# Performance work log

Hardware: AMD Instinct MI355X
Metric: run time of the kernel (lower is better)

Reference implementation:

```python
import jax, jax.numpy as jnp
import numpy as np

SEQ_LEN = 12
B = 1024
NG = 32            # scenes
G = B // NG        # pedestrians per scene
E = 64             # embedding_dim
H = 128            # h_dim
PP = 512           # mlp_pre_pool hidden
BOT = 1024         # bottleneck_dim
MLPD = 1024        # mlp_dim


def _w(key, fan_in, shape):
    return jax.random.normal(key, shape, jnp.float32) / np.sqrt(fan_in)


def setup_inputs():
    key = jax.random.key(0)
    ks = jax.random.split(key, 16)
    starts = jnp.arange(NG, dtype=jnp.int32) * G
    inp = {
        'last_pos': jax.random.normal(ks[0], (B, 2), jnp.float32),
        'last_pos_rel': jax.random.normal(ks[1], (B, 2), jnp.float32) * 0.1,
        'decoder_h': jax.random.normal(ks[2], (1, B, H), jnp.float32) * 0.1,
        'decoder_c': jax.random.normal(ks[3], (1, B, H), jnp.float32) * 0.1,
        'seq_start_end': jnp.stack([starts, starts + G], axis=1),
        'W_emb': _w(ks[4], 2, (2, E)), 'b_emb': jnp.zeros((E,), jnp.float32),
        'W_ih': _w(ks[5], E, (4 * H, E)), 'b_ih': jnp.zeros((4 * H,), jnp.float32),
        'W_hh': _w(ks[6], H, (4 * H, H)), 'b_hh': jnp.zeros((4 * H,), jnp.float32),
        'W_h2p': _w(ks[7], H, (H, 2)), 'b_h2p': jnp.zeros((2,), jnp.float32),
        'W_sp': _w(ks[8], 2, (2, E)), 'b_sp': jnp.zeros((E,), jnp.float32),
        'W_pp1': _w(ks[9], E + H, (E + H, PP)), 'b_pp1': jnp.zeros((PP,), jnp.float32),
        'W_pp2': _w(ks[10], PP, (PP, BOT)), 'b_pp2': jnp.zeros((BOT,), jnp.float32),
        'W_m1': _w(ks[11], H + BOT, (H + BOT, MLPD)), 'b_m1': jnp.zeros((MLPD,), jnp.float32),
        'W_m2': _w(ks[12], MLPD, (MLPD, H)), 'b_m2': jnp.zeros((H,), jnp.float32),
    }
    return inp


def _forward(last_pos, last_pos_rel, h0, c0,
             W_emb, b_emb, W_ih, b_ih, W_hh, b_hh, W_h2p, b_h2p,
             W_sp, b_sp, W_pp1, b_pp1, W_pp2, b_pp2, W_m1, b_m1, W_m2, b_m2):
    relu = jax.nn.relu

    def pool_net(h, pos):
        # PoolHiddenNet over NG contiguous equal-size groups of G peds.
        hg = h.reshape(NG, G, H)
        pg = pos.reshape(NG, G, 2)
        # rel[g, i, j] = pos_j - pos_i  (matches repeat/tile ordering in torch code)
        rel = pg[:, None, :, :] - pg[:, :, None, :]          # [NG,G,G,2]
        emb = rel @ W_sp + b_sp                               # [NG,G,G,E]
        hj = jnp.broadcast_to(hg[:, None, :, :], (NG, G, G, H))
        x = jnp.concatenate([emb, hj], axis=-1)               # [NG,G,G,E+H]
        x = relu(x @ W_pp1 + b_pp1)
        x = relu(x @ W_pp2 + b_pp2)                           # [NG,G,G,BOT]
        return jnp.max(x, axis=2).reshape(B, BOT)             # max over neighbors j

    def lstm_cell(x, h, c):
        gates = x @ W_ih.T + b_ih + h @ W_hh.T + b_hh
        i, f, g, o = jnp.split(gates, 4, axis=-1)
        c2 = jax.nn.sigmoid(f) * c + jax.nn.sigmoid(i) * jnp.tanh(g)
        h2 = jax.nn.sigmoid(o) * jnp.tanh(c2)
        return h2, c2

    dec_in0 = last_pos_rel @ W_emb + b_emb

    def step(carry, _):
        lp, din, h, c = carry
        h, c = lstm_cell(din, h, c)
        rel_pos = h @ W_h2p + b_h2p                           # [B,2]
        curr_pos = rel_pos + lp
        pool_h = pool_net(h, curr_pos)                        # [B,BOT]
        hcat = jnp.concatenate([h, pool_h], axis=1)
        h = relu(relu(hcat @ W_m1 + b_m1) @ W_m2 + b_m2)      # refreshed decoder_h
        din = rel_pos @ W_emb + b_emb
        return (curr_pos, din, h, c), rel_pos

    (_, _, h_fin, _), pred = jax.lax.scan(
        step, (last_pos, dec_in0, h0, c0), None, length=SEQ_LEN)
    return pred, h_fin[None]                                  # [T,B,2], [1,B,H]


def reference(last_pos, last_pos_rel, decoder_h, decoder_c, seq_start_end,
              W_emb, b_emb, W_ih, b_ih, W_hh, b_hh, W_h2p, b_h2p,
              W_sp, b_sp, W_pp1, b_pp1, W_pp2, b_pp2, W_m1, b_m1, W_m2, b_m2):
    del seq_start_end  # uniform contiguous groups encoded statically (NG, G)
    return _forward(last_pos, last_pos_rel, decoder_h[0], decoder_c[0],
                    W_emb, b_emb, W_ih, b_ih, W_hh, b_hh, W_h2p, b_h2p,
                    W_sp, b_sp, W_pp1, b_pp1, W_pp2, b_pp2, W_m1, b_m1, W_m2, b_m2)
```

## Files before the change

kernel.cpp:

```cpp
#include <hip/hip_runtime.h>
#include <math.h>

#define T_SEQ 12

typedef __bf16 bf16x8 __attribute__((ext_vector_type(8)));
typedef float f32x4 __attribute__((ext_vector_type(4)));
typedef unsigned short u16x8 __attribute__((ext_vector_type(8)));

static __device__ __forceinline__ unsigned short bf16bits(float x) {
  return __builtin_bit_cast(unsigned short, (__bf16)x);
}

enum : int {
  OFF_LP    = 0,
  OFF_DIN   = 2048,
  OFF_C     = 198656,
  OFF_HDEC  = 329728,
  OFF_WC    = 460800,
  OFF_BC    = 461824,
  OFF_PW    = 462336,
  OFF_AA    = 986624,
  OFF_WP2T  = 1510912,
  OFF_WM1T  = 1773056,
  OFF_HCATB = 2362880,
  OFF_WM2TB = 2952704,
  OFF_MIDB  = 3018240,
  OFF_WIHT  = 3542528,
  OFF_WHHT  = 3575296,
  OFF_WFRAG = 3640832
};

#define SWZP(byte, row) ((byte) ^ (((row) & 7) << 4))

__global__ __launch_bounds__(256) void k_setup(
    const float* __restrict__ last_pos, const float* __restrict__ lpr,
    const float* __restrict__ dh, const float* __restrict__ dc,
    const float* __restrict__ W_emb, const float* __restrict__ b_emb,
    float* __restrict__ lp, float* __restrict__ din,
    float* __restrict__ h_dec, float* __restrict__ c) {
  int idx = blockIdx.x * 256 + threadIdx.x;
  if (idx < 2048) lp[idx] = last_pos[idx];
  h_dec[idx] = dh[idx];
  c[idx] = dc[idx];
  if (idx < 65536) {
    int b = idx >> 6, e = idx & 63;
    din[idx] = lpr[b*2] * W_emb[e] + lpr[b*2+1] * W_emb[64+e] + b_emb[e];
  }
}

__global__ __launch_bounds__(256) void k_wc(
    const float* __restrict__ W_sp, const float* __restrict__ b_sp,
    const float* __restrict__ W_pp1, const float* __restrict__ b_pp1,
    float* __restrict__ Wc, float* __restrict__ bc) {
  int n = blockIdx.x * 256 + threadIdx.x;
  if (n >= 512) return;
  float a0 = 0.f, a1 = 0.f, ab = 0.f;
#pragma unroll 8
  for (int k = 0; k < 64; k++) {
    float w = W_pp1[k*512 + n];
    a0 += W_sp[k] * w;
    a1 += W_sp[64+k] * w;
    ab += b_sp[k] * w;
  }
  Wc[n] = a0; Wc[512+n] = a1; bc[n] = ab + b_pp1[n];
}

__global__ __launch_bounds__(256) void k_tcvt(
    const float* __restrict__ src, unsigned short* __restrict__ dst,
    int R, int C) {
  __shared__ float t[32][33];
  const int bx = blockIdx.x * 32, by = blockIdx.y * 32;
  const int tx = threadIdx.x & 31, ty = threadIdx.x >> 5;
#pragma unroll
  for (int i = 0; i < 32; i += 8) t[ty+i][tx] = src[(size_t)(by+ty+i)*C + bx+tx];
  __syncthreads();
#pragma unroll
  for (int i = 0; i < 32; i += 8)
    dst[(size_t)(bx+ty+i)*R + by+tx] = bf16bits(t[tx][ty+i]);
}

__global__ __launch_bounds__(256) void k_t32(
    const float* __restrict__ src, float* __restrict__ dst, int R, int C) {
  __shared__ float t[32][33];
  const int bx = blockIdx.x * 32, by = blockIdx.y * 32;
  const int tx = threadIdx.x & 31, ty = threadIdx.x >> 5;
#pragma unroll
  for (int i = 0; i < 32; i += 8) t[ty+i][tx] = src[(size_t)(by+ty+i)*C + bx+tx];
  __syncthreads();
#pragma unroll
  for (int i = 0; i < 32; i += 8)
    dst[(size_t)(bx+ty+i)*R + by+tx] = t[tx][ty+i];
}

__global__ __launch_bounds__(256) void k_frag(
    const unsigned short* __restrict__ Wp2t, unsigned short* __restrict__ Wfrag) {
  const int tid = blockIdx.x * 256 + threadIdx.x;
  const int fid = tid >> 6, l = tid & 63;
  const int nbb = fid >> 4, ks = fid & 15;
  u16x8 v = *(const u16x8*)(Wp2t + (size_t)(nbb*16 + (l & 15))*512 +
                            ks*32 + (l >> 4)*8);
  *(u16x8*)(Wfrag + (size_t)tid*8) = v;
}

__global__ __launch_bounds__(512) void k_step1(
    float* __restrict__ din, const float* __restrict__ h_dec,
    float* __restrict__ cst, unsigned short* __restrict__ hcatB,
    float* __restrict__ lp, float* __restrict__ pred,
    const float* __restrict__ Wiht, const float* __restrict__ b_ih,
    const float* __restrict__ Whht, const float* __restrict__ b_hh,
    const float* __restrict__ W_h2p, const float* __restrict__ b_h2p,
    const float* __restrict__ W_emb, const float* __restrict__ b_emb,
    const float* __restrict__ W1b, const float* __restrict__ Wc,
    const float* __restrict__ bc,
    float* __restrict__ PW, float* __restrict__ Aa, int t) {
  const int b0 = blockIdx.x * 4;
  const int tid = threadIdx.x;
  __shared__ float xh[4*192];
  __shared__ float gl[4*512];
  __shared__ float hbuf[4*128];
  __shared__ float relS[8], curS[8];

  for (int i = tid; i < 768; i += 512) {
    int r = i / 192, k = i - r*192;
    xh[i] = (k < 64) ? din[(b0+r)*64 + k] : h_dec[(b0+r)*128 + k - 64];
  }
  __syncthreads();
  {
    const int n = tid;
    float bias = b_ih[n] + b_hh[n];
    float acc[4] = {bias, bias, bias, bias};
#pragma unroll 8
    for (int k = 0; k < 64; k++) {
      float wv = Wiht[k*512 + n];
#pragma unroll
      for (int r = 0; r < 4; r++) acc[r] += xh[r*192 + k] * wv;
    }
#pragma unroll 8
    for (int k = 0; k < 128; k++) {
      float wv = Whht[k*512 + n];
#pragma unroll
      for (int r = 0; r < 4; r++) acc[r] += xh[r*192 + 64 + k] * wv;
    }
#pragma unroll
    for (int r = 0; r < 4; r++) gl[r*512 + n] = acc[r];
  }
  __syncthreads();
  {
    int r = tid >> 7, hh = tid & 127;
    float ig = gl[r*512 + hh],       fg = gl[r*512 + 128 + hh];
    float gg = gl[r*512 + 256 + hh], og = gl[r*512 + 384 + hh];
    ig = 1.f/(1.f+expf(-ig)); fg = 1.f/(1.f+expf(-fg));
    gg = tanhf(gg);           og = 1.f/(1.f+expf(-og));
    int row = b0 + r;
    float c2 = fg * cst[row*128 + hh] + ig * gg;
    float h2 = og * tanhf(c2);
    cst[row*128 + hh] = c2;
    hbuf[r*128 + hh] = h2;
    hcatB[(size_t)row*1152 + hh] = bf16bits(h2);
  }
  __syncthreads();
  if (tid < 128) {
    int r = tid >> 5, col = (tid >> 4) & 1, l16 = tid & 15;
    float s = 0.f;
    for (int k = l16; k < 128; k += 16) s += hbuf[r*128 + k] * W_h2p[k*2 + col];
#pragma unroll
    for (int off = 8; off > 0; off >>= 1) s += __shfl_xor(s, off);
    if (l16 == 0) {
      float rel = s + b_h2p[col];
      float old = lp[(b0+r)*2 + col];
      relS[r*2 + col] = rel;
      curS[r*2 + col] = old + rel;
      lp[(b0+r)*2 + col] = old + rel;
      pred[t*2048 + (b0+r)*2 + col] = rel;
    }
  }
  __syncthreads();
  if (tid < 256) {
    int r = tid >> 6, e = tid & 63;
    din[(b0+r)*64 + e] = relS[r*2]*W_emb[e] + relS[r*2+1]*W_emb[64+e] + b_emb[e];
  }
  {
    const int n = tid;
    float acc[4] = {0.f, 0.f, 0.f, 0.f};
#pragma unroll 4
    for (int k = 0; k < 128; k++) {
      float wv = W1b[k*512 + n];
#pragma unroll
      for (int r = 0; r < 4; r++) acc[r] += hbuf[r*128 + k] * wv;
    }
    float wc0 = Wc[n], wc1 = Wc[512+n], bcv = bc[n];
#pragma unroll
    for (int r = 0; r < 4; r++) {
      float pw = curS[r*2]*wc0 + curS[r*2+1]*wc1;
      PW[(size_t)(b0+r)*512 + n] = pw;
      Aa[(size_t)(b0+r)*512 + n] = acc[r] + pw + bcv;
    }
  }
}

__global__ __launch_bounds__(512) void k_pool8(
    const float* __restrict__ Aa, const float* __restrict__ PW,
    const unsigned short* __restrict__ Wfrag, const float* __restrict__ bp2,
    unsigned short* __restrict__ hcatB) {
  const int bid = blockIdx.x;
  const int mt = (bid >> 3) & 7;
  const int g  = (bid & 7) + ((bid >> 6) << 3);
  const int tid = threadIdx.x, lane = tid & 63, w = tid >> 6;
  const int wr = w >> 2, wc = w & 3;
  const int l15 = lane & 15, lhi = lane >> 4;
  __shared__ __align__(128) char lds[163840];
  char* As = lds;
  char* B0 = lds + 131072;
  char* B1 = lds + 131072 + 16384;

  {
    const int ke = lane * 8;
#pragma unroll 4
    for (int rr = 0; rr < 16; rr++) {
      const int r = rr * 8 + w;
      const int j = r & 31, ii = r >> 5;
      const float* aRow = Aa + (size_t)(g*32 + j)*512 + ke;
      const float* pRow = PW + (size_t)(g*32 + mt*4 + ii)*512 + ke;
      float4 a0 = *(const float4*)aRow;
      float4 a1 = *(const float4*)(aRow + 4);
      float4 p0 = *(const float4*)pRow;
      float4 p1 = *(const float4*)(pRow + 4);
      bf16x8 y;
      y[0] = (__bf16)fmaxf(a0.x - p0.x, 0.f);
      y[1] = (__bf16)fmaxf(a0.y - p0.y, 0.f);
      y[2] = (__bf16)fmaxf(a0.z - p0.z, 0.f);
      y[3] = (__bf16)fmaxf(a0.w - p0.w, 0.f);
      y[4] = (__bf16)fmaxf(a1.x - p1.x, 0.f);
      y[5] = (__bf16)fmaxf(a1.y - p1.y, 0.f);
      y[6] = (__bf16)fmaxf(a1.z - p1.z, 0.f);
      y[7] = (__bf16)fmaxf(a1.w - p1.w, 0.f);
      *(bf16x8*)(As + SWZP(r*1024 + lane*16, r)) = y;
    }
  }

  const int u0 = tid, u1 = tid + 512;
  const size_t gfo0 = (size_t)((u0 >> 6) * 16) * 512 + (u0 & 63) * 8;
  const size_t gfo1 = (size_t)((u1 >> 6) * 16) * 512 + (u1 & 63) * 8;

  {
    u16x8 s0 = *(const u16x8*)(Wfrag + gfo0);
    u16x8 s1 = *(const u16x8*)(Wfrag + gfo1);
    *(u16x8*)(B0 + u0*16) = s0;
    *(u16x8*)(B0 + u1*16) = s1;
  }
  u16x8 r0, r1;
  {
    const size_t base = (size_t)512;
    r0 = *(const u16x8*)(Wfrag + base + gfo0);
    r1 = *(const u16x8*)(Wfrag + base + gfo1);
  }
  __syncthreads();

  for (int nt = 0; nt < 4; nt++) {
    f32x4 acc[4][4] = {};
#pragma unroll 4
    for (int k0 = 0; k0 < 16; k0++) {
      const int q = nt*16 + k0;
      char* Bcur = (q & 1) ? B1 : B0;
      char* Bnxt = (q & 1) ? B0 : B1;
      if (q < 63) {
        *(u16x8*)(Bnxt + u0*16) = r0;
        *(u16x8*)(Bnxt + u1*16) = r1;
      }
      if (q < 62) {
        const int q2 = q + 2;
        const size_t base = (size_t)((q2 >> 4) * 256 + (q2 & 15)) * 512;
        r0 = *(const u16x8*)(Wfrag + base + gfo0);
        r1 = *(const u16x8*)(Wfrag + base + gfo1);
      }
      bf16x8 af[4], bfr[4];
#pragma unroll
      for (int mf = 0; mf < 4; mf++) {
        const int row = wr*64 + mf*16 + l15;
        af[mf] = *(const bf16x8*)(As + SWZP(row*1024 + k0*64 + lhi*16, row));
      }
#pragma unroll
      for (int nf = 0; nf < 4; nf++)
        bfr[nf] = *(const bf16x8*)(Bcur + (wc*4 + nf)*1024 + lane*16);
#pragma unroll
      for (int mf = 0; mf < 4; mf++)
#pragma unroll
        for (int nf = 0; nf < 4; nf++)
          acc[mf][nf] = __builtin_amdgcn_mfma_f32_16x16x32_bf16(
              af[mf], bfr[nf], acc[mf][nf], 0, 0, 0);
      __syncthreads();
    }
#pragma unroll
    for (int isub = 0; isub < 2; isub++)
#pragma unroll
      for (int nf = 0; nf < 4; nf++) {
        f32x4 v0 = acc[isub*2][nf], v1 = acc[isub*2 + 1][nf];
        float mx = fmaxf(fmaxf(fmaxf(v0[0], v0[1]), fmaxf(v0[2], v0[3])),
                         fmaxf(fmaxf(v1[0], v1[1]), fmaxf(v1[2], v1[3])));
        mx = fmaxf(mx, __shfl_xor(mx, 16));
        mx = fmaxf(mx, __shfl_xor(mx, 32));
        if (lane < 16) {
          const int n = nt*256 + wc*64 + nf*16 + lane;
          const int i = mt*4 + wr*2 + isub;
          hcatB[(size_t)(g*32 + i)*1152 + 128 + n] =
              bf16bits(fmaxf(mx + bp2[n], 0.f));
        }
      }
  }
}

__global__ __launch_bounds__(256) void k_m1k(
    const unsigned short* __restrict__ A, const unsigned short* __restrict__ Bw,
    const float* __restrict__ bias, unsigned short* __restrict__ outB) {
  const int nt = blockIdx.x, mt = blockIdx.y;
  const int tid = threadIdx.x, lane = tid & 63, w = tid >> 6;
  const int l15 = lane & 15, lhi = lane >> 4;
  __shared__ __align__(128) char lds[65536];
  const unsigned short* aSrc = A  + (size_t)(mt*64)*1152;
  const unsigned short* bSrc = Bw + (size_t)(nt*64)*1152;

  u16x8 rg[8];
#pragma unroll
  for (int p = 0; p < 8; p++) {
    const int u = tid + p*256;
    const int isB = u >> 10, v = u & 1023;
    const int row = v >> 4, slot = v & 15;
    u16x8 val = *(const u16x8*)((isB ? bSrc : aSrc) + (size_t)row*1152 + slot*8);
    *(u16x8*)(lds + isB*16384 + SWZP(row*256 + slot*16, row)) = val;
  }
#pragma unroll
  for (int p = 0; p < 8; p++) {
    const int u = tid + p*256;
    const int isB = u >> 10, v = u & 1023;
    const int row = v >> 4, slot = v & 15;
    rg[p] = *(const u16x8*)((isB ? bSrc : aSrc) + (size_t)row*1152 + 128 + slot*8);
  }
  __syncthreads();

  f32x4 acc[4][4] = {};
  for (int c = 0; c < 9; c++) {
    const int cur = (c & 1) * 32768;
    const int nxt = 32768 - cur;
    if (c < 8) {
#pragma unroll
      for (int p = 0; p < 8; p++) {
        const int u = tid + p*256;
        const int isB = u >> 10, v = u & 1023;
        const int row = v >> 4, slot = v & 15;
        *(u16x8*)(lds + nxt + isB*16384 + SWZP(row*256 + slot*16, row)) = rg[p];
      }
    }
    if (c < 7) {
#pragma unroll
      for (int p = 0; p < 8; p++) {
        const int u = tid + p*256;
        const int isB = u >> 10, v = u & 1023;
        const int row = v >> 4, slot = v & 15;
        rg[p] = *(const u16x8*)((isB ? bSrc : aSrc) + (size_t)row*1152 +
                                (c+2)*128 + slot*8);
      }
    }
    bf16x8 af[4], bf[4];
#pragma unroll
    for (int mf = 0; mf < 4; mf++) {
      const int row = mf*16 + l15;
      af[mf] = *(const bf16x8*)(lds + cur + SWZP(row*256 + w*64 + lhi*16, row));
    }
#pragma unroll
    for (int nf = 0; nf < 4; nf++) {
      const int row = nf*16 + l15;
      bf[nf] = *(const bf16x8*)(lds + cur + 16384 +
                                SWZP(row*256 + w*64 + lhi*16, row));
    }
#pragma unroll
    for (int mf = 0; mf < 4; mf++)
#pragma unroll
      for (int nf = 0; nf < 4; nf++)
        acc[mf][nf] = __builtin_amdgcn_mfma_f32_16x16x32_bf16(
            af[mf], bf[nf], acc[mf][nf], 0, 0, 0);
    __syncthreads();
  }

#pragma unroll
  for (int mf = 0; mf < 4; mf++)
#pragma unroll
    for (int nf = 0; nf < 4; nf++)
      *(f32x4*)(lds + w*16384 + (mf*4 + nf)*1024 + lane*16) = acc[mf][nf];
  __syncthreads();
#pragma unroll
  for (int pi = 0; pi < 4; pi++) {
    const int p = w*4 + pi;
    f32x4 s = *(const f32x4*)(lds + p*1024 + lane*16);
#pragma unroll
    for (int wv = 1; wv < 4; wv++) {
      f32x4 q = *(const f32x4*)(lds + wv*16384 + p*1024 + lane*16);
      s[0] += q[0]; s[1] += q[1]; s[2] += q[2]; s[3] += q[3];
    }
    const int col = nt*64 + (p & 3)*16 + l15;
    const float bv = bias[col];
#pragma unroll
    for (int r = 0; r < 4; r++) {
      const int row = mt*64 + (p >> 2)*16 + lhi*4 + r;
      outB[(size_t)row*1024 + col] = bf16bits(fmaxf(s[r] + bv, 0.f));
    }
  }
}

__global__ __launch_bounds__(256) void k_m2k(
    const unsigned short* __restrict__ A, const unsigned short* __restrict__ Bw,
    const float* __restrict__ bias, float* __restrict__ hd) {
  const int nt = blockIdx.x, mt = blockIdx.y;
  const int tid = threadIdx.x, lane = tid & 63, w = tid >> 6;
  const int l15 = lane & 15, lhi = lane >> 4;
  __shared__ __align__(128) char lds[49152];
  const unsigned short* aSrc = A  + (size_t)(mt*32)*1024;
  const unsigned short* bSrc = Bw + (size_t)(nt*64)*1024;

  u16x8 rg[6];
#pragma unroll
  for (int p = 0; p < 6; p++) {
    const int u = tid + p*256;
    const int isB = (u >= 512);
    const int v = isB ? (u - 512) : u;
    const int row = v >> 4, slot = v & 15;
    u16x8 val = *(const u16x8*)((isB ? bSrc : aSrc) + (size_t)row*1024 + slot*8);
    *(u16x8*)(lds + isB*8192 + SWZP(row*256 + slot*16, row)) = val;
  }
#pragma unroll
  for (int p = 0; p < 6; p++) {
    const int u = tid + p*256;
    const int isB = (u >= 512);
    const int v = isB ? (u - 512) : u;
    const int row = v >> 4, slot = v & 15;
    rg[p] = *(const u16x8*)((isB ? bSrc : aSrc) + (size_t)row*1024 + 128 + slot*8);
  }
  __syncthreads();

  f32x4 acc[2][4] = {};
  for (int c = 0; c < 8; c++) {
    const int cur = (c & 1) * 24576;
    const int nxt = 24576 - cur;
    if (c < 7) {
#pragma unroll
      for (int p = 0; p < 6; p++) {
        const int u = tid + p*256;
        const int isB = (u >= 512);
        const int v = isB ? (u - 512) : u;
        const int row = v >> 4, slot = v & 15;
        *(u16x8*)(lds + nxt + isB*8192 + SWZP(row*256 + slot*16, row)) = rg[p];
      }
    }
    if (c < 6) {
#pragma unroll
      for (int p = 0; p < 6; p++) {
        const int u = tid + p*256;
        const int isB = (u >= 512);
        const int v = isB ? (u - 512) : u;
        const int row = v >> 4, slot = v & 15;
        rg[p] = *(const u16x8*)((isB ? bSrc : aSrc) + (size_t)row*1024 +
                                (c+2)*128 + slot*8);
      }
    }
    bf16x8 af[2], bf[4];
#pragma unroll
    for (int mf = 0; mf < 2; mf++) {
      const int row = mf*16 + l15;
      af[mf] = *(const bf16x8*)(lds + cur + SWZP(row*256 + w*64 + lhi*16, row));
    }
#pragma unroll
    for (int nf = 0; nf < 4; nf++) {
      const int row = nf*16 + l15;
      bf[nf] = *(const bf16x8*)(lds + cur + 8192 +
                                SWZP(row*256 + w*64 + lhi*16, row));
    }
#pragma unroll
    for (int mf = 0; mf < 2; mf++)
#pragma unroll
      for (int nf = 0; nf < 4; nf++)
        acc[mf][nf] = __builtin_amdgcn_mfma_f32_16x16x32_bf16(
            af[mf], bf[nf], acc[mf][nf], 0, 0, 0);
    __syncthreads();
  }

#pragma unroll
  for (int mf = 0; mf < 2; mf++)
#pragma unroll
    for (int nf = 0; nf < 4; nf++)
      *(f32x4*)(lds + w*8192 + (mf*4 + nf)*1024 + lane*16) = acc[mf][nf];
  __syncthreads();
#pragma unroll
  for (int pi = 0; pi < 2; pi++) {
    const int p = w*2 + pi;
    f32x4 s = *(const f32x4*)(lds + p*1024 + lane*16);
#pragma unroll
    for (int wv = 1; wv < 4; wv++) {
      f32x4 q = *(const f32x4*)(lds + wv*8192 + p*1024 + lane*16);
      s[0] += q[0]; s[1] += q[1]; s[2] += q[2]; s[3] += q[3];
    }
    const int col = nt*64 + (p & 3)*16 + l15;
    const float bv = bias[col];
#pragma unroll
    for (int r = 0; r < 4; r++) {
      const int row = mt*32 + (p >> 2)*16 + lhi*4 + r;
      hd[(size_t)row*128 + col] = fmaxf(s[r] + bv, 0.f);
    }
  }
}

__global__ __launch_bounds__(256) void k_hfin(const float* __restrict__ h_dec,
                                              float* __restrict__ out) {
  int idx = blockIdx.x * 256 + threadIdx.x;
  if (idx < 131072) out[24576 + idx] = h_dec[idx];
}

extern "C" void kernel_launch(void* const* d_in, const int* in_sizes, int n_in,
                              void* d_out, int out_size, void* d_ws, size_t ws_size,
                              hipStream_t stream) {
  const float* last_pos = (const float*)d_in[0];
  const float* lpr      = (const float*)d_in[1];
  const float* dh       = (const float*)d_in[2];
  const float* dc       = (const float*)d_in[3];
  const float* W_emb = (const float*)d_in[5];
  const float* b_emb = (const float*)d_in[6];
  const float* W_ih  = (const float*)d_in[7];
  const float* b_ih  = (const float*)d_in[8];
  const float* W_hh  = (const float*)d_in[9];
  const float* b_hh  = (const float*)d_in[10];
  const float* W_h2p = (const float*)d_in[11];
  const float* b_h2p = (const float*)d_in[12];
  const float* W_sp  = (const float*)d_in[13];
  const float* b_sp  = (const float*)d_in[14];
  const float* W_pp1 = (const float*)d_in[15];
  const float* b_pp1 = (const float*)d_in[16];
  const float* W_pp2 = (const float*)d_in[17];
  const float* b_pp2 = (const float*)d_in[18];
  const float* W_m1  = (const float*)d_in[19];
  const float* b_m1  = (const float*)d_in[20];
  const float* W_m2  = (const float*)d_in[21];
  const float* b_m2  = (const float*)d_in[22];

  float* ws    = (float*)d_ws;
  float* lp    = ws + OFF_LP;
  float* din   = ws + OFF_DIN;
  float* cst   = ws + OFF_C;
  float* h_dec = ws + OFF_HDEC;
  float* Wc    = ws + OFF_WC;
  float* bc    = ws + OFF_BC;
  float* PW    = ws + OFF_PW;
  float* Aa    = ws + OFF_AA;
  unsigned short* Wp2t  = (unsigned short*)(ws + OFF_WP2T);
  unsigned short* Wm1t  = (unsigned short*)(ws + OFF_WM1T);
  unsigned short* hcatB = (unsigned short*)(ws + OFF_HCATB);
  unsigned short* Wm2tB = (unsigned short*)(ws + OFF_WM2TB);
  unsigned short* midB  = (unsigned short*)(ws + OFF_MIDB);
  float* Wiht  = ws + OFF_WIHT;
  float* Whht  = ws + OFF_WHHT;
  unsigned short* Wfrag = (unsigned short*)(ws + OFF_WFRAG);
  float* out   = (float*)d_out;

  k_setup<<<512, 256, 0, stream>>>(last_pos, lpr, dh, dc, W_emb, b_emb, lp, din, h_dec, cst);
  k_wc<<<2, 256, 0, stream>>>(W_sp, b_sp, W_pp1, b_pp1, Wc, bc);
  { dim3 gt(32, 16); k_tcvt<<<gt, 256, 0, stream>>>(W_pp2, Wp2t, 512, 1024); }
  { dim3 gt(32, 36); k_tcvt<<<gt, 256, 0, stream>>>(W_m1, Wm1t, 1152, 1024); }
  { dim3 gt(4, 32);  k_tcvt<<<gt, 256, 0, stream>>>(W_m2, Wm2tB, 1024, 128); }
  { dim3 gt(2, 16);  k_t32<<<gt, 256, 0, stream>>>(W_ih, Wiht, 512, 64); }
  { dim3 gt(4, 16);  k_t32<<<gt, 256, 0, stream>>>(W_hh, Whht, 512, 128); }
  k_frag<<<256, 256, 0, stream>>>(Wp2t, Wfrag);

  for (int t = 0; t < T_SEQ; t++) {
    k_step1<<<256, 512, 0, stream>>>(din, h_dec, cst, hcatB, lp, out,
                                     Wiht, b_ih, Whht, b_hh, W_h2p, b_h2p,
                                     W_emb, b_emb, W_pp1 + 64*512, Wc, bc,
                                     PW, Aa, t);
    k_pool8<<<256, 512, 0, stream>>>(Aa, PW, Wfrag, b_pp2, hcatB);
    { dim3 gm(16, 16); k_m1k<<<gm, 256, 0, stream>>>(hcatB, Wm1t, b_m1, midB); }
    { dim3 gm(2, 32);  k_m2k<<<gm, 256, 0, stream>>>(midB, Wm2tB, b_m2, h_dec); }
  }
  k_hfin<<<512, 256, 0, stream>>>(h_dec, out);
}
```

Baseline: 994.9 us.

## Fuse per-step kernels into one persistent cooperative kernel with grid syncs

Replaces the 48 per-timestep launches (LSTM step, pooling GEMM, two MLP GEMMs) and the final copy with one cooperative kernel of 256 blocks that loops over timesteps and uses grid.sync between stages. The m1/m2 GEMMs are re-tiled to fit the 256-block, 512-thread grid. The goal is to remove launch overhead and inter-kernel gaps. In exchange, each block must use 160KB LDS and only one block fits per CU, so the GEMM stages run with a fixed grid shape and grid-wide barriers, which may lower occupancy or efficiency for the smaller GEMMs.

```diff
diff --git a/kernel.cpp b/kernel.cpp
--- a/kernel.cpp
+++ b/kernel.cpp
@@ -1,5 +1,8 @@
 #include <hip/hip_runtime.h>
+#include <hip/hip_cooperative_groups.h>
 #include <math.h>
+
+namespace cg = cooperative_groups;
 
 #define T_SEQ 12
 
@@ -102,415 +105,404 @@
   *(u16x8*)(Wfrag + (size_t)tid*8) = v;
 }
 
-__global__ __launch_bounds__(512) void k_step1(
-    float* __restrict__ din, const float* __restrict__ h_dec,
-    float* __restrict__ cst, unsigned short* __restrict__ hcatB,
-    float* __restrict__ lp, float* __restrict__ pred,
-    const float* __restrict__ Wiht, const float* __restrict__ b_ih,
-    const float* __restrict__ Whht, const float* __restrict__ b_hh,
-    const float* __restrict__ W_h2p, const float* __restrict__ b_h2p,
-    const float* __restrict__ W_emb, const float* __restrict__ b_emb,
-    const float* __restrict__ W1b, const float* __restrict__ Wc,
-    const float* __restrict__ bc,
-    float* __restrict__ PW, float* __restrict__ Aa, int t) {
-  const int b0 = blockIdx.x * 4;
-  const int tid = threadIdx.x;
-  __shared__ float xh[4*192];
-  __shared__ float gl[4*512];
-  __shared__ float hbuf[4*128];
-  __shared__ float relS[8], curS[8];
-
-  for (int i = tid; i < 768; i += 512) {
-    int r = i / 192, k = i - r*192;
-    xh[i] = (k < 64) ? din[(b0+r)*64 + k] : h_dec[(b0+r)*128 + k - 64];
-  }
-  __syncthreads();
-  {
-    const int n = tid;
-    float bias = b_ih[n] + b_hh[n];
-    float acc[4] = {bias, bias, bias, bias};
-#pragma unroll 8
-    for (int k = 0; k < 64; k++) {
-      float wv = Wiht[k*512 + n];
-#pragma unroll
-      for (int r = 0; r < 4; r++) acc[r] += xh[r*192 + k] * wv;
-    }
-#pragma unroll 8
-    for (int k = 0; k < 128; k++) {
-      float wv = Whht[k*512 + n];
-#pragma unroll
-      for (int r = 0; r < 4; r++) acc[r] += xh[r*192 + 64 + k] * wv;
-    }
-#pragma unroll
-    for (int r = 0; r < 4; r++) gl[r*512 + n] = acc[r];
-  }
-  __syncthreads();
-  {
-    int r = tid >> 7, hh = tid & 127;
-    float ig = gl[r*512 + hh],       fg = gl[r*512 + 128 + hh];
-    float gg = gl[r*512 + 256 + hh], og = gl[r*512 + 384 + hh];
-    ig = 1.f/(1.f+expf(-ig)); fg = 1.f/(1.f+expf(-fg));
-    gg = tanhf(gg);           og = 1.f/(1.f+expf(-og));
-    int row = b0 + r;
-    float c2 = fg * cst[row*128 + hh] + ig * gg;
-    float h2 = og * tanhf(c2);
-    cst[row*128 + hh] = c2;
-    hbuf[r*128 + hh] = h2;
-    hcatB[(size_t)row*1152 + hh] = bf16bits(h2);
-  }
-  __syncthreads();
-  if (tid < 128) {
-    int r = tid >> 5, col = (tid >> 4) & 1, l16 = tid & 15;
-    float s = 0.f;
-    for (int k = l16; k < 128; k += 16) s += hbuf[r*128 + k] * W_h2p[k*2 + col];
-#pragma unroll
-    for (int off = 8; off > 0; off >>= 1) s += __shfl_xor(s, off);
-    if (l16 == 0) {
-      float rel = s + b_h2p[col];
-      float old = lp[(b0+r)*2 + col];
-      relS[r*2 + col] = rel;
-      curS[r*2 + col] = old + rel;
-      lp[(b0+r)*2 + col] = old + rel;
-      pred[t*2048 + (b0+r)*2 + col] = rel;
-    }
-  }
-  __syncthreads();
-  if (tid < 256) {
-    int r = tid >> 6, e = tid & 63;
-    din[(b0+r)*64 + e] = relS[r*2]*W_emb[e] + relS[r*2+1]*W_emb[64+e] + b_emb[e];
-  }
-  {
-    const int n = tid;
-    float acc[4] = {0.f, 0.f, 0.f, 0.f};
-#pragma unroll 4
-    for (int k = 0; k < 128; k++) {
-      float wv = W1b[k*512 + n];
-#pragma unroll
-      for (int r = 0; r < 4; r++) acc[r] += hbuf[r*128 + k] * wv;
-    }
-    float wc0 = Wc[n], wc1 = Wc[512+n], bcv = bc[n];
-#pragma unroll
-    for (int r = 0; r < 4; r++) {
-      float pw = curS[r*2]*wc0 + curS[r*2+1]*wc1;
-      PW[(size_t)(b0+r)*512 + n] = pw;
-      Aa[(size_t)(b0+r)*512 + n] = acc[r] + pw + bcv;
-    }
-  }
-}
-
-__global__ __launch_bounds__(512) void k_pool8(
-    const float* __restrict__ Aa, const float* __restrict__ PW,
-    const unsigned short* __restrict__ Wfrag, const float* __restrict__ bp2,
-    unsigned short* __restrict__ hcatB) {
+__global__ void __launch_bounds__(512)
+k_mega(float* din, float* cst, float* h_dec, unsigned short* hcatB,
+       float* lp, float* out,
+       const float* Wiht, const float* b_ih,
+       const float* Whht, const float* b_hh,
+       const float* W_h2p, const float* b_h2p,
+       const float* W_emb, const float* b_emb,
+       const float* W1b, const float* Wc, const float* bc,
+       float* PW, float* Aa,
+       const unsigned short* Wfrag, const float* bp2,
+       const unsigned short* Wm1t, const float* b_m1, unsigned short* midB,
+       const unsigned short* Wm2tB, const float* b_m2) {
+  cg::grid_group grid = cg::this_grid();
+  __shared__ __align__(128) char smem[163840];
   const int bid = blockIdx.x;
-  const int mt = (bid >> 3) & 7;
-  const int g  = (bid & 7) + ((bid >> 6) << 3);
-  const int tid = threadIdx.x, lane = tid & 63, w = tid >> 6;
-  const int wr = w >> 2, wc = w & 3;
-  const int l15 = lane & 15, lhi = lane >> 4;
-  __shared__ __align__(128) char lds[163840];
-  char* As = lds;
-  char* B0 = lds + 131072;
-  char* B1 = lds + 131072 + 16384;
-
-  {
-    const int ke = lane * 8;
-#pragma unroll 4
-    for (int rr = 0; rr < 16; rr++) {
-      const int r = rr * 8 + w;
-      const int j = r & 31, ii = r >> 5;
-      const float* aRow = Aa + (size_t)(g*32 + j)*512 + ke;
-      const float* pRow = PW + (size_t)(g*32 + mt*4 + ii)*512 + ke;
-      float4 a0 = *(const float4*)aRow;
-      float4 a1 = *(const float4*)(aRow + 4);
-      float4 p0 = *(const float4*)pRow;
-      float4 p1 = *(const float4*)(pRow + 4);
-      bf16x8 y;
-      y[0] = (__bf16)fmaxf(a0.x - p0.x, 0.f);
-      y[1] = (__bf16)fmaxf(a0.y - p0.y, 0.f);
-      y[2] = (__bf16)fmaxf(a0.z - p0.z, 0.f);
-      y[3] = (__bf16)fmaxf(a0.w - p0.w, 0.f);
-      y[4] = (__bf16)fmaxf(a1.x - p1.x, 0.f);
-      y[5] = (__bf16)fmaxf(a1.y - p1.y, 0.f);
-      y[6] = (__bf16)fmaxf(a1.z - p1.z, 0.f);
-      y[7] = (__bf16)fmaxf(a1.w - p1.w, 0.f);
-      *(bf16x8*)(As + SWZP(r*1024 + lane*16, r)) = y;
-    }
-  }
-
-  const int u0 = tid, u1 = tid + 512;
-  const size_t gfo0 = (size_t)((u0 >> 6) * 16) * 512 + (u0 & 63) * 8;
-  const size_t gfo1 = (size_t)((u1 >> 6) * 16) * 512 + (u1 & 63) * 8;
-
-  {
-    u16x8 s0 = *(const u16x8*)(Wfrag + gfo0);
-    u16x8 s1 = *(const u16x8*)(Wfrag + gfo1);
-    *(u16x8*)(B0 + u0*16) = s0;
-    *(u16x8*)(B0 + u1*16) = s1;
-  }
-  u16x8 r0, r1;
-  {
-    const size_t base = (size_t)512;
-    r0 = *(const u16x8*)(Wfrag + base + gfo0);
-    r1 = *(const u16x8*)(Wfrag + base + gfo1);
-  }
-  __syncthreads();
-
-  for (int nt = 0; nt < 4; nt++) {
-    f32x4 acc[4][4] = {};
-#pragma unroll 4
-    for (int k0 = 0; k0 < 16; k0++) {
-      const int q = nt*16 + k0;
-      char* Bcur = (q & 1) ? B1 : B0;
-      char* Bnxt = (q & 1) ? B0 : B1;
-      if (q < 63) {
-        *(u16x8*)(Bnxt + u0*16) = r0;
-        *(u16x8*)(Bnxt + u1*16) = r1;
-      }
-      if (q < 62) {
-        const int q2 = q + 2;
-        const size_t base = (size_t)((q2 >> 4) * 256 + (q2 & 15)) * 512;
-        r0 = *(const u16x8*)(Wfrag + base + gfo0);
-        r1 = *(const u16x8*)(Wfrag + base + gfo1);
-      }
-      bf16x8 af[4], bfr[4];
-#pragma unroll
-      for (int mf = 0; mf < 4; mf++) {
-        const int row = wr*64 + mf*16 + l15;
-        af[mf] = *(const bf16x8*)(As + SWZP(row*1024 + k0*64 + lhi*16, row));
-      }
-#pragma unroll
-      for (int nf = 0; nf < 4; nf++)
-        bfr[nf] = *(const bf16x8*)(Bcur + (wc*4 + nf)*1024 + lane*16);
-#pragma unroll
-      for (int mf = 0; mf < 4; mf++)
-#pragma unroll
-        for (int nf = 0; nf < 4; nf++)
-          acc[mf][nf] = __builtin_amdgcn_mfma_f32_16x16x32_bf16(
-              af[mf], bfr[nf], acc[mf][nf], 0, 0, 0);
-      __syncthreads();
-    }
-#pragma unroll
-    for (int isub = 0; isub < 2; isub++)
-#pragma unroll
-      for (int nf = 0; nf < 4; nf++) {
-        f32x4 v0 = acc[isub*2][nf], v1 = acc[isub*2 + 1][nf];
-        float mx = fmaxf(fmaxf(fmaxf(v0[0], v0[1]), fmaxf(v0[2], v0[3])),
-                         fmaxf(fmaxf(v1[0], v1[1]), fmaxf(v1[2], v1[3])));
-        mx = fmaxf(mx, __shfl_xor(mx, 16));
-        mx = fmaxf(mx, __shfl_xor(mx, 32));
-        if (lane < 16) {
-          const int n = nt*256 + wc*64 + nf*16 + lane;
-          const int i = mt*4 + wr*2 + isub;
-          hcatB[(size_t)(g*32 + i)*1152 + 128 + n] =
-              bf16bits(fmaxf(mx + bp2[n], 0.f));
-        }
-      }
-  }
-}
-
-__global__ __launch_bounds__(256) void k_m1k(
-    const unsigned short* __restrict__ A, const unsigned short* __restrict__ Bw,
-    const float* __restrict__ bias, unsigned short* __restrict__ outB) {
-  const int nt = blockIdx.x, mt = blockIdx.y;
   const int tid = threadIdx.x, lane = tid & 63, w = tid >> 6;
   const int l15 = lane & 15, lhi = lane >> 4;
-  __shared__ __align__(128) char lds[65536];
-  const unsigned short* aSrc = A  + (size_t)(mt*64)*1152;
-  const unsigned short* bSrc = Bw + (size_t)(nt*64)*1152;
-
-  u16x8 rg[8];
-#pragma unroll
-  for (int p = 0; p < 8; p++) {
-    const int u = tid + p*256;
-    const int isB = u >> 10, v = u & 1023;
-    const int row = v >> 4, slot = v & 15;
-    u16x8 val = *(const u16x8*)((isB ? bSrc : aSrc) + (size_t)row*1152 + slot*8);
-    *(u16x8*)(lds + isB*16384 + SWZP(row*256 + slot*16, row)) = val;
-  }
-#pragma unroll
-  for (int p = 0; p < 8; p++) {
-    const int u = tid + p*256;
-    const int isB = u >> 10, v = u & 1023;
-    const int row = v >> 4, slot = v & 15;
-    rg[p] = *(const u16x8*)((isB ? bSrc : aSrc) + (size_t)row*1152 + 128 + slot*8);
-  }
-  __syncthreads();
-
-  f32x4 acc[4][4] = {};
-  for (int c = 0; c < 9; c++) {
-    const int cur = (c & 1) * 32768;
-    const int nxt = 32768 - cur;
-    if (c < 8) {
-#pragma unroll
-      for (int p = 0; p < 8; p++) {
-        const int u = tid + p*256;
+
+  for (int t = 0; t < T_SEQ; t++) {
+    {
+      float* xh   = (float*)smem;
+      float* gl   = xh + 768;
+      float* hbuf = gl + 2048;
+      float* relS = hbuf + 512;
+      float* curS = relS + 8;
+      const int b0 = bid * 4;
+      for (int i = tid; i < 768; i += 512) {
+        int r = i / 192, k = i - r*192;
+        xh[i] = (k < 64) ? din[(b0+r)*64 + k] : h_dec[(b0+r)*128 + k - 64];
+      }
+      __syncthreads();
+      {
+        const int n = tid;
+        float bias = b_ih[n] + b_hh[n];
+        float acc[4] = {bias, bias, bias, bias};
+#pragma unroll 8
+        for (int k = 0; k < 64; k++) {
+          float wv = Wiht[k*512 + n];
+#pragma unroll
+          for (int r = 0; r < 4; r++) acc[r] += xh[r*192 + k] * wv;
+        }
+#pragma unroll 8
+        for (int k = 0; k < 128; k++) {
+          float wv = Whht[k*512 + n];
+#pragma unroll
+          for (int r = 0; r < 4; r++) acc[r] += xh[r*192 + 64 + k] * wv;
+        }
+#pragma unroll
+        for (int r = 0; r < 4; r++) gl[r*512 + n] = acc[r];
+      }
+      __syncthreads();
+      {
+        int r = tid >> 7, hh = tid & 127;
+        float ig = gl[r*512 + hh],       fg = gl[r*512 + 128 + hh];
+        float gg = gl[r*512 + 256 + hh], og = gl[r*512 + 384 + hh];
+        ig = 1.f/(1.f+expf(-ig)); fg = 1.f/(1.f+expf(-fg));
+        gg = tanhf(gg);           og = 1.f/(1.f+expf(-og));
+        int row = b0 + r;
+        float c2 = fg * cst[row*128 + hh] + ig * gg;
+        float h2 = og * tanhf(c2);
+        cst[row*128 + hh] = c2;
+        hbuf[r*128 + hh] = h2;
+        hcatB[(size_t)row*1152 + hh] = bf16bits(h2);
+      }
+      __syncthreads();
+      if (tid < 128) {
+        int r = tid >> 5, col = (tid >> 4) & 1, l16 = tid & 15;
+        float s = 0.f;
+        for (int k = l16; k < 128; k += 16) s += hbuf[r*128 + k] * W_h2p[k*2 + col];
+#pragma unroll
+        for (int off = 8; off > 0; off >>= 1) s += __shfl_xor(s, off);
+        if (l16 == 0) {
+          float rel = s + b_h2p[col];
+          float old = lp[(b0+r)*2 + col];
+          relS[r*2 + col] = rel;
+          curS[r*2 + col] = old + rel;
+          lp[(b0+r)*2 + col] = old + rel;
+          out[t*2048 + (b0+r)*2 + col] = rel;
+        }
+      }
+      __syncthreads();
+      if (tid < 256) {
+        int r = tid >> 6, e = tid & 63;
+        din[(b0+r)*64 + e] = relS[r*2]*W_emb[e] + relS[r*2+1]*W_emb[64+e] + b_emb[e];
+      }
+      {
+        const int n = tid;
+        float acc[4] = {0.f, 0.f, 0.f, 0.f};
+#pragma unroll 4
+        for (int k = 0; k < 128; k++) {
+          float wv = W1b[k*512 + n];
+#pragma unroll
+          for (int r = 0; r < 4; r++) acc[r] += hbuf[r*128 + k] * wv;
+        }
+        float wc0 = Wc[n], wc1 = Wc[512+n], bcv = bc[n];
+#pragma unroll
+        for (int r = 0; r < 4; r++) {
+          float pw = curS[r*2]*wc0 + curS[r*2+1]*wc1;
+          PW[(size_t)(b0+r)*512 + n] = pw;
+          Aa[(size_t)(b0+r)*512 + n] = acc[r] + pw + bcv;
+        }
+      }
+    }
+    grid.sync();
+
+    {
+      const int mt = (bid >> 3) & 7;
+      const int g  = (bid & 7) + ((bid >> 6) << 3);
+      const int wr = w >> 2, wcn = w & 3;
+      char* As = smem;
+      char* B0 = smem + 131072;
+      char* B1 = smem + 131072 + 16384;
+      {
+        const int ke = lane * 8;
+#pragma unroll 4
+        for (int rr = 0; rr < 16; rr++) {
+          const int r = rr * 8 + w;
+          const int j = r & 31, ii = r >> 5;
+          const float* aRow = Aa + (size_t)(g*32 + j)*512 + ke;
+          const float* pRow = PW + (size_t)(g*32 + mt*4 + ii)*512 + ke;
+          float4 a0 = *(const float4*)aRow;
+          float4 a1 = *(const float4*)(aRow + 4);
+          float4 p0 = *(const float4*)pRow;
+          float4 p1 = *(const float4*)(pRow + 4);
+          bf16x8 y;
+          y[0] = (__bf16)fmaxf(a0.x - p0.x, 0.f);
+          y[1] = (__bf16)fmaxf(a0.y - p0.y, 0.f);
+          y[2] = (__bf16)fmaxf(a0.z - p0.z, 0.f);
+          y[3] = (__bf16)fmaxf(a0.w - p0.w, 0.f);
+          y[4] = (__bf16)fmaxf(a1.x - p1.x, 0.f);
+          y[5] = (__bf16)fmaxf(a1.y - p1.y, 0.f);
+          y[6] = (__bf16)fmaxf(a1.z - p1.z, 0.f);
+          y[7] = (__bf16)fmaxf(a1.w - p1.w, 0.f);
+          *(bf16x8*)(As + SWZP(r*1024 + lane*16, r)) = y;
+        }
+      }
+      const int u0 = tid, u1 = tid + 512;
+      const size_t gfo0 = (size_t)((u0 >> 6) * 16) * 512 + (u0 & 63) * 8;
+      const size_t gfo1 = (size_t)((u1 >> 6) * 16) * 512 + (u1 & 63) * 8;
+      {
+        u16x8 s0 = *(const u16x8*)(Wfrag + gfo0);
+        u16x8 s1 = *(const u16x8*)(Wfrag + gfo1);
+        *(u16x8*)(B0 + u0*16) = s0;
+        *(u16x8*)(B0 + u1*16) = s1;
+      }
+      u16x8 r0, r1;
+      {
+        r0 = *(const u16x8*)(Wfrag + 512 + gfo0);
+        r1 = *(const u16x8*)(Wfrag + 512 + gfo1);
+      }
+      __syncthreads();
+      for (int nt2 = 0; nt2 < 4; nt2++) {
+        f32x4 acc[4][4] = {};
+        for (int k0 = 0; k0 < 16; k0++) {
+          const int q = nt2*16 + k0;
+          char* Bcur = (q & 1) ? B1 : B0;
+          char* Bnxt = (q & 1) ? B0 : B1;
+          if (q < 63) {
+            *(u16x8*)(Bnxt + u0*16) = r0;
+            *(u16x8*)(Bnxt + u1*16) = r1;
+          }
+          if (q < 62) {
+            const int q2 = q + 2;
+            const size_t base = (size_t)((q2 >> 4) * 256 + (q2 & 15)) * 512;
+            r0 = *(const u16x8*)(Wfrag + base + gfo0);
+            r1 = *(const u16x8*)(Wfrag + base + gfo1);
+          }
+          bf16x8 af[4], bfr[4];
+#pragma unroll
+          for (int mf = 0; mf < 4; mf++) {
+            const int row = wr*64 + mf*16 + l15;
+            af[mf] = *(const bf16x8*)(As + SWZP(row*1024 + k0*64 + lhi*16, row));
+          }
+#pragma unroll
+          for (int nf = 0; nf < 4; nf++)
+            bfr[nf] = *(const bf16x8*)(Bcur + (wcn*4 + nf)*1024 + lane*16);
+#pragma unroll
+          for (int mf = 0; mf < 4; mf++)
+#pragma unroll
+            for (int nf = 0; nf < 4; nf++)
+              acc[mf][nf] = __builtin_amdgcn_mfma_f32_16x16x32_bf16(
+                  af[mf], bfr[nf], acc[mf][nf], 0, 0, 0);
+          __syncthreads();
+        }
+#pragma unroll
+        for (int isub = 0; isub < 2; isub++)
+#pragma unroll
+          for (int nf = 0; nf < 4; nf++) {
+            f32x4 v0 = acc[isub*2][nf], v1 = acc[isub*2 + 1][nf];
+            float mx = fmaxf(fmaxf(fmaxf(v0[0], v0[1]), fmaxf(v0[2], v0[3])),
+                             fmaxf(fmaxf(v1[0], v1[1]), fmaxf(v1[2], v1[3])));
+            mx = fmaxf(mx, __shfl_xor(mx, 16));
+            mx = fmaxf(mx, __shfl_xor(mx, 32));
+            if (lane < 16) {
+              const int n = nt2*256 + wcn*64 + nf*16 + lane;
+              const int i = mt*4 + wr*2 + isub;
+              hcatB[(size_t)(g*32 + i)*1152 + 128 + n] =
+                  bf16bits(fmaxf(mx + bp2[n], 0.f));
+            }
+          }
+      }
+    }
+    grid.sync();
+
+    {
+      const int nt = bid & 15, mt = bid >> 4;
+      const unsigned short* aSrc = hcatB + (size_t)(mt*64)*1152;
+      const unsigned short* bSrc = Wm1t + (size_t)(nt*64)*1152;
+      const int wk = w >> 1, wn = w & 1;
+      u16x8 rg[4];
+#pragma unroll
+      for (int p = 0; p < 4; p++) {
+        const int u = tid + p*512;
         const int isB = u >> 10, v = u & 1023;
         const int row = v >> 4, slot = v & 15;
-        *(u16x8*)(lds + nxt + isB*16384 + SWZP(row*256 + slot*16, row)) = rg[p];
-      }
-    }
-    if (c < 7) {
-#pragma unroll
-      for (int p = 0; p < 8; p++) {
-        const int u = tid + p*256;
+        u16x8 val = *(const u16x8*)((isB ? bSrc : aSrc) + (size_t)row*1152 + slot*8);
+        *(u16x8*)(smem + isB*16384 + SWZP(row*256 + slot*16, row)) = val;
+      }
+#pragma unroll
+      for (int p = 0; p < 4; p++) {
+        const int u = tid + p*512;
         const int isB = u >> 10, v = u & 1023;
         const int row = v >> 4, slot = v & 15;
-        rg[p] = *(const u16x8*)((isB ? bSrc : aSrc) + (size_t)row*1152 +
-                                (c+2)*128 + slot*8);
+        rg[p] = *(const u16x8*)((isB ? bSrc : aSrc) + (size_t)row*1152 + 128 + slot*8);
+      }
+      __syncthreads();
+      f32x4 acc[4][2] = {};
+      for (int c = 0; c < 9; c++) {
+        const int cur = (c & 1) * 32768;
+        const int nxt = 32768 - cur;
+        if (c < 8) {
+#pragma unroll
+          for (int p = 0; p < 4; p++) {
+            const int u = tid + p*512;
+            const int isB = u >> 10, v = u & 1023;
+            const int row = v >> 4, slot = v & 15;
+            *(u16x8*)(smem + nxt + isB*16384 + SWZP(row*256 + slot*16, row)) = rg[p];
+          }
+        }
+        if (c < 7) {
+#pragma unroll
+          for (int p = 0; p < 4; p++) {
+            const int u = tid + p*512;
+            const int isB = u >> 10, v = u & 1023;
+            const int row = v >> 4, slot = v & 15;
+            rg[p] = *(const u16x8*)((isB ? bSrc : aSrc) + (size_t)row*1152 +
+                                    (c+2)*128 + slot*8);
+          }
+        }
+        bf16x8 af[4], bf[2];
+#pragma unroll
+        for (int mf = 0; mf < 4; mf++) {
+          const int row = mf*16 + l15;
+          af[mf] = *(const bf16x8*)(smem + cur +
+                                    SWZP(row*256 + wk*64 + lhi*16, row));
+        }
+#pragma unroll
+        for (int nf = 0; nf < 2; nf++) {
+          const int row = wn*32 + nf*16 + l15;
+          bf[nf] = *(const bf16x8*)(smem + cur + 16384 +
+                                    SWZP(row*256 + wk*64 + lhi*16, row));
+        }
+#pragma unroll
+        for (int mf = 0; mf < 4; mf++)
+#pragma unroll
+          for (int nf = 0; nf < 2; nf++)
+            acc[mf][nf] = __builtin_amdgcn_mfma_f32_16x16x32_bf16(
+                af[mf], bf[nf], acc[mf][nf], 0, 0, 0);
+        __syncthreads();
+      }
+#pragma unroll
+      for (int mf = 0; mf < 4; mf++)
+#pragma unroll
+        for (int nf = 0; nf < 2; nf++)
+          *(f32x4*)(smem + (w*8 + mf*2 + nf)*1024 + lane*16) = acc[mf][nf];
+      __syncthreads();
+#pragma unroll
+      for (int pi = 0; pi < 2; pi++) {
+        const int p = w*2 + pi;
+        const int mf = p >> 2, nfg = p & 3;
+        f32x4 s = {0.f, 0.f, 0.f, 0.f};
+#pragma unroll
+        for (int wkk = 0; wkk < 4; wkk++) {
+          const int src = (wkk*2 + (nfg >> 1))*8 + mf*2 + (nfg & 1);
+          f32x4 q = *(const f32x4*)(smem + src*1024 + lane*16);
+          s[0] += q[0]; s[1] += q[1]; s[2] += q[2]; s[3] += q[3];
+        }
+        const int col = nt*64 + nfg*16 + l15;
+        const float bv = b_m1[col];
+#pragma unroll
+        for (int r = 0; r < 4; r++) {
+          const int row = mt*64 + mf*16 + lhi*4 + r;
+          midB[(size_t)row*1024 + col] = bf16bits(fmaxf(s[r] + bv, 0.f));
+        }
       }
     }
-    bf16x8 af[4], bf[4];
-#pragma unroll
-    for (int mf = 0; mf < 4; mf++) {
-      const int row = mf*16 + l15;
-      af[mf] = *(const bf16x8*)(lds + cur + SWZP(row*256 + w*64 + lhi*16, row));
+    grid.sync();
+
+    if (bid < 64) {
+      const int nt = bid & 1, mt = bid >> 1;
+      const unsigned short* aSrc = midB  + (size_t)(mt*32)*1024;
+      const unsigned short* bSrc = Wm2tB + (size_t)(nt*64)*1024;
+      u16x8 rg[6];
+#pragma unroll
+      for (int p = 0; p < 6; p++) {
+        const int u = tid + p*512;
+        const int isB = (u >= 1024);
+        const int v = isB ? (u - 1024) : u;
+        const int row = v >> 5, slot = v & 31;
+        u16x8 val = *(const u16x8*)((isB ? bSrc : aSrc) + (size_t)row*1024 + slot*8);
+        *(u16x8*)(smem + isB*16384 + SWZP(row*512 + slot*16, row)) = val;
+      }
+#pragma unroll
+      for (int p = 0; p < 6; p++) {
+        const int u = tid + p*512;
+        const int isB = (u >= 1024);
+        const int v = isB ? (u - 1024) : u;
+        const int row = v >> 5, slot = v & 31;
+        rg[p] = *(const u16x8*)((isB ? bSrc : aSrc) + (size_t)row*1024 + 256 + slot*8);
+      }
+      __syncthreads();
+      f32x4 acc[2][4] = {};
+      for (int c = 0; c < 4; c++) {
+        const int cur = (c & 1) * 49152;
+        const int nxt = 49152 - cur;
+        if (c < 3) {
+#pragma unroll
+          for (int p = 0; p < 6; p++) {
+            const int u = tid + p*512;
+            const int isB = (u >= 1024);
+            const int v = isB ? (u - 1024) : u;
+            const int row = v >> 5, slot = v & 31;
+            *(u16x8*)(smem + nxt + isB*16384 + SWZP(row*512 + slot*16, row)) = rg[p];
+          }
+        }
+        if (c < 2) {
+#pragma unroll
+          for (int p = 0; p < 6; p++) {
+            const int u = tid + p*512;
+            const int isB = (u >= 1024);
+            const int v = isB ? (u - 1024) : u;
+            const int row = v >> 5, slot = v & 31;
+            rg[p] = *(const u16x8*)((isB ? bSrc : aSrc) + (size_t)row*1024 +
+                                    (c+2)*256 + slot*8);
+          }
+        }
+        bf16x8 af[2], bf[4];
+#pragma unroll
+        for (int mf = 0; mf < 2; mf++) {
+          const int row = mf*16 + l15;
+          af[mf] = *(const bf16x8*)(smem + cur +
+                                    SWZP(row*512 + w*64 + lhi*16, row));
+        }
+#pragma unroll
+        for (int nf = 0; nf < 4; nf++) {
+          const int row = nf*16 + l15;
+          bf[nf] = *(const bf16x8*)(smem + cur + 16384 +
+                                    SWZP(row*512 + w*64 + lhi*16, row));
+        }
+#pragma unroll
+        for (int mf = 0; mf < 2; mf++)
+#pragma unroll
+          for (int nf = 0; nf < 4; nf++)
+            acc[mf][nf] = __builtin_amdgcn_mfma_f32_16x16x32_bf16(
+                af[mf], bf[nf], acc[mf][nf], 0, 0, 0);
+        __syncthreads();
+      }
+#pragma unroll
+      for (int mf = 0; mf < 2; mf++)
+#pragma unroll
+        for (int nf = 0; nf < 4; nf++)
+          *(f32x4*)(smem + (w*8 + mf*4 + nf)*1024 + lane*16) = acc[mf][nf];
+      __syncthreads();
+      {
+        const int p = w;
+        const int mf = p >> 2, nf = p & 3;
+        f32x4 s = {0.f, 0.f, 0.f, 0.f};
+#pragma unroll
+        for (int wv = 0; wv < 8; wv++) {
+          f32x4 q = *(const f32x4*)(smem + (wv*8 + p)*1024 + lane*16);
+          s[0] += q[0]; s[1] += q[1]; s[2] += q[2]; s[3] += q[3];
+        }
+        const int col = nt*64 + nf*16 + l15;
+        const float bv = b_m2[col];
+#pragma unroll
+        for (int r = 0; r < 4; r++) {
+          const int row = mt*32 + mf*16 + lhi*4 + r;
+          h_dec[(size_t)row*128 + col] = fmaxf(s[r] + bv, 0.f);
+        }
+      }
     }
-#pragma unroll
-    for (int nf = 0; nf < 4; nf++) {
-      const int row = nf*16 + l15;
-      bf[nf] = *(const bf16x8*)(lds + cur + 16384 +
-                                SWZP(row*256 + w*64 + lhi*16, row));
-    }
-#pragma unroll
-    for (int mf = 0; mf < 4; mf++)
-#pragma unroll
-      for (int nf = 0; nf < 4; nf++)
-        acc[mf][nf] = __builtin_amdgcn_mfma_f32_16x16x32_bf16(
-            af[mf], bf[nf], acc[mf][nf], 0, 0, 0);
-    __syncthreads();
+    grid.sync();
   }
 
-#pragma unroll
-  for (int mf = 0; mf < 4; mf++)
-#pragma unroll
-    for (int nf = 0; nf < 4; nf++)
-      *(f32x4*)(lds + w*16384 + (mf*4 + nf)*1024 + lane*16) = acc[mf][nf];
-  __syncthreads();
-#pragma unroll
-  for (int pi = 0; pi < 4; pi++) {
-    const int p = w*4 + pi;
-    f32x4 s = *(const f32x4*)(lds + p*1024 + lane*16);
-#pragma unroll
-    for (int wv = 1; wv < 4; wv++) {
-      f32x4 q = *(const f32x4*)(lds + wv*16384 + p*1024 + lane*16);
-      s[0] += q[0]; s[1] += q[1]; s[2] += q[2]; s[3] += q[3];
-    }
-    const int col = nt*64 + (p & 3)*16 + l15;
-    const float bv = bias[col];
-#pragma unroll
-    for (int r = 0; r < 4; r++) {
-      const int row = mt*64 + (p >> 2)*16 + lhi*4 + r;
-      outB[(size_t)row*1024 + col] = bf16bits(fmaxf(s[r] + bv, 0.f));
-    }
+  {
+    const int idx = bid * 512 + tid;
+    out[24576 + idx] = h_dec[idx];
   }
-}
-
-__global__ __launch_bounds__(256) void k_m2k(
-    const unsigned short* __restrict__ A, const unsigned short* __restrict__ Bw,
-    const float* __restrict__ bias, float* __restrict__ hd) {
-  const int nt = blockIdx.x, mt = blockIdx.y;
-  const int tid = threadIdx.x, lane = tid & 63, w = tid >> 6;
-  const int l15 = lane & 15, lhi = lane >> 4;
-  __shared__ __align__(128) char lds[49152];
-  const unsigned short* aSrc = A  + (size_t)(mt*32)*1024;
-  const unsigned short* bSrc = Bw + (size_t)(nt*64)*1024;
-
-  u16x8 rg[6];
-#pragma unroll
-  for (int p = 0; p < 6; p++) {
-    const int u = tid + p*256;
-    const int isB = (u >= 512);
-    const int v = isB ? (u - 512) : u;
-    const int row = v >> 4, slot = v & 15;
-    u16x8 val = *(const u16x8*)((isB ? bSrc : aSrc) + (size_t)row*1024 + slot*8);
-    *(u16x8*)(lds + isB*8192 + SWZP(row*256 + slot*16, row)) = val;
-  }
-#pragma unroll
-  for (int p = 0; p < 6; p++) {
-    const int u = tid + p*256;
-    const int isB = (u >= 512);
-    const int v = isB ? (u - 512) : u;
-    const int row = v >> 4, slot = v & 15;
-    rg[p] = *(const u16x8*)((isB ? bSrc : aSrc) + (size_t)row*1024 + 128 + slot*8);
-  }
-  __syncthreads();
-
-  f32x4 acc[2][4] = {};
-  for (int c = 0; c < 8; c++) {
-    const int cur = (c & 1) * 24576;
-    const int nxt = 24576 - cur;
-    if (c < 7) {
-#pragma unroll
-      for (int p = 0; p < 6; p++) {
-        const int u = tid + p*256;
-        const int isB = (u >= 512);
-        const int v = isB ? (u - 512) : u;
-        const int row = v >> 4, slot = v & 15;
-        *(u16x8*)(lds + nxt + isB*8192 + SWZP(row*256 + slot*16, row)) = rg[p];
-      }
-    }
-    if (c < 6) {
-#pragma unroll
-      for (int p = 0; p < 6; p++) {
-        const int u = tid + p*256;
-        const int isB = (u >= 512);
-        const int v = isB ? (u - 512) : u;
-        const int row = v >> 4, slot = v & 15;
-        rg[p] = *(const u16x8*)((isB ? bSrc : aSrc) + (size_t)row*1024 +
-                                (c+2)*128 + slot*8);
-      }
-    }
-    bf16x8 af[2], bf[4];
-#pragma unroll
-    for (int mf = 0; mf < 2; mf++) {
-      const int row = mf*16 + l15;
-      af[mf] = *(const bf16x8*)(lds + cur + SWZP(row*256 + w*64 + lhi*16, row));
-    }
-#pragma unroll
-    for (int nf = 0; nf < 4; nf++) {
-      const int row = nf*16 + l15;
-      bf[nf] = *(const bf16x8*)(lds + cur + 8192 +
-                                SWZP(row*256 + w*64 + lhi*16, row));
-    }
-#pragma unroll
-    for (int mf = 0; mf < 2; mf++)
-#pragma unroll
-      for (int nf = 0; nf < 4; nf++)
-        acc[mf][nf] = __builtin_amdgcn_mfma_f32_16x16x32_bf16(
-            af[mf], bf[nf], acc[mf][nf], 0, 0, 0);
-    __syncthreads();
-  }
-
-#pragma unroll
-  for (int mf = 0; mf < 2; mf++)
-#pragma unroll
-    for (int nf = 0; nf < 4; nf++)
-      *(f32x4*)(lds + w*8192 + (mf*4 + nf)*1024 + lane*16) = acc[mf][nf];
-  __syncthreads();
-#pragma unroll
-  for (int pi = 0; pi < 2; pi++) {
-    const int p = w*2 + pi;
-    f32x4 s = *(const f32x4*)(lds + p*1024 + lane*16);
-#pragma unroll
-    for (int wv = 1; wv < 4; wv++) {
-      f32x4 q = *(const f32x4*)(lds + wv*8192 + p*1024 + lane*16);
-      s[0] += q[0]; s[1] += q[1]; s[2] += q[2]; s[3] += q[3];
-    }
-    const int col = nt*64 + (p & 3)*16 + l15;
-    const float bv = bias[col];
-#pragma unroll
-    for (int r = 0; r < 4; r++) {
-      const int row = mt*32 + (p >> 2)*16 + lhi*4 + r;
-      hd[(size_t)row*128 + col] = fmaxf(s[r] + bv, 0.f);
-    }
-  }
-}
-
-__global__ __launch_bounds__(256) void k_hfin(const float* __restrict__ h_dec,
-                                              float* __restrict__ out) {
-  int idx = blockIdx.x * 256 + threadIdx.x;
-  if (idx < 131072) out[24576 + idx] = h_dec[idx];
 }
 
 extern "C" void kernel_launch(void* const* d_in, const int* in_sizes, int n_in,
@@ -557,6 +549,7 @@
   float* Whht  = ws + OFF_WHHT;
   unsigned short* Wfrag = (unsigned short*)(ws + OFF_WFRAG);
   float* out   = (float*)d_out;
+  const float* W1b = W_pp1 + 64*512;
 
   k_setup<<<512, 256, 0, stream>>>(last_pos, lpr, dh, dc, W_emb, b_emb, lp, din, h_dec, cst);
   k_wc<<<2, 256, 0, stream>>>(W_sp, b_sp, W_pp1, b_pp1, Wc, bc);
@@ -567,14 +560,16 @@
   { dim3 gt(4, 16);  k_t32<<<gt, 256, 0, stream>>>(W_hh, Whht, 512, 128); }
   k_frag<<<256, 256, 0, stream>>>(Wp2t, Wfrag);
 
-  for (int t = 0; t < T_SEQ; t++) {
-    k_step1<<<256, 512, 0, stream>>>(din, h_dec, cst, hcatB, lp, out,
-                                     Wiht, b_ih, Whht, b_hh, W_h2p, b_h2p,
-                                     W_emb, b_emb, W_pp1 + 64*512, Wc, bc,
-                                     PW, Aa, t);
-    k_pool8<<<256, 512, 0, stream>>>(Aa, PW, Wfrag, b_pp2, hcatB);
-    { dim3 gm(16, 16); k_m1k<<<gm, 256, 0, stream>>>(hcatB, Wm1t, b_m1, midB); }
-    { dim3 gm(2, 32);  k_m2k<<<gm, 256, 0, stream>>>(midB, Wm2tB, b_m2, h_dec); }
-  }
-  k_hfin<<<512, 256, 0, stream>>>(h_dec, out);
-}
+  void* args[] = {
+    (void*)&din, (void*)&cst, (void*)&h_dec, (void*)&hcatB,
+    (void*)&lp, (void*)&out,
+    (void*)&Wiht, (void*)&b_ih, (void*)&Whht, (void*)&b_hh,
+    (void*)&W_h2p, (void*)&b_h2p, (void*)&W_emb, (void*)&b_emb,
+    (void*)&W1b, (void*)&Wc, (void*)&bc,
+    (void*)&PW, (void*)&Aa,
+    (void*)&Wfrag, (void*)&b_pp2,
+    (void*)&Wm1t, (void*)&b_m1, (void*)&midB,
+    (void*)&Wm2tB, (void*)&b_m2
+  };
+  hipLaunchCooperativeKernel((void*)k_mega, dim3(256), dim3(512), args, 0, stream);
+}
```

After: 2.330 ms. 2.34x slower.
